# Kernel optimization log

Measured on AMD Instinct MI355X. Metric: run time of the kernel, lower is better.

Reference implementation:

```python
import jax, jax.numpy as jnp
from jax import lax
import numpy as np

INPUT_SIZE, HIDDEN_SIZE, OUTPUT_SIZE = 256, 2048, 128
NUM_STEPS = 8192
ALPHA = 0.1


def setup_inputs() -> dict:
    key = jax.random.key(0)
    ks = jax.random.split(key, 8)
    s_i = 1.0 / np.sqrt(INPUT_SIZE)
    s_h = 1.0 / np.sqrt(HIDDEN_SIZE)
    return {
        "input_sig": jax.random.normal(ks[0], (INPUT_SIZE, NUM_STEPS), jnp.float32),
        "rate": jax.random.uniform(ks[1], (HIDDEN_SIZE,), jnp.float32, -1.0, 1.0),
        "Wi": jax.random.uniform(ks[2], (HIDDEN_SIZE, INPUT_SIZE), jnp.float32, -s_i, s_i),
        "bi": jax.random.uniform(ks[3], (HIDDEN_SIZE,), jnp.float32, -s_i, s_i),
        "Wh": jax.random.uniform(ks[4], (HIDDEN_SIZE, HIDDEN_SIZE), jnp.float32, -s_h, s_h),
        "bh": jax.random.uniform(ks[5], (HIDDEN_SIZE,), jnp.float32, -s_h, s_h),
        "Wo": jax.random.uniform(ks[6], (OUTPUT_SIZE, HIDDEN_SIZE), jnp.float32, -s_h, s_h),
        "bo": jax.random.uniform(ks[7], (OUTPUT_SIZE,), jnp.float32, -s_h, s_h),
    }


def reference(input_sig, rate, Wi, bi, Wh, bh, Wo, bo):
    # Precompute input projection for all steps at once: (T, H)
    xproj = input_sig.T @ Wi.T + bi  # einsum 'ti,hi->th'

    def step(r, xp):
        r_new = jnp.tanh(xp + r @ Wh.T + bh)
        r = (1.0 - ALPHA) * r + ALPHA * r_new
        return r, r

    _, rates = lax.scan(step, rate, xproj)  # rates: (T, H)
    rate_all = rates.T                      # (H, T), matches torch stack(dim=1)
    logits = rates @ Wo.T + bo              # (T, O)
    output = jax.nn.log_softmax(logits.T, axis=0)  # LogSoftmax over classes
    return output, rate_all
```

## Files before the change

### kernel.cpp

```cpp
#include <hip/hip_runtime.h>
#include <math.h>

#define T_STEPS 8192
#define HID     2048
#define IN_SZ   256
#define OUT_SZ  128
#define NBLK    128
#define NTHR    512
#define RPB     16
#define SCRUB   0xFFFFFFFF00000000ull

typedef unsigned long long u64;
typedef unsigned int u32;
typedef __attribute__((ext_vector_type(4))) u32 u32x4;


__global__ void k_init(const float* __restrict__ rate, u64* ring) {
    int i = blockIdx.x * blockDim.x + threadIdx.x;
    if (i < HID) {
        ring[i] = (u64)__float_as_uint(rate[i]);
        ring[HID + i]     = SCRUB;
        ring[2 * HID + i] = SCRUB;
    }
}

__global__ void __launch_bounds__(256) k_xproj(const float* __restrict__ sig,
                                               const float* __restrict__ Wi,
                                               const float* __restrict__ bi,
                                               float* __restrict__ out2) {
    __shared__ float wl[32 * IN_SZ];
    const int tid = threadIdx.x;
    const int t0 = blockIdx.x * 512;
    const int h0 = blockIdx.y * 32;

    {
        const float4* s4 = (const float4*)(Wi + (size_t)h0 * IN_SZ);
        float4* d4 = (float4*)wl;
        #pragma unroll
        for (int k = 0; k < 8; ++k) d4[tid + k * 256] = s4[tid + k * 256];
    }
    __syncthreads();

    const int t1 = t0 + tid, t2 = t1 + 256;
    float acc1[32], acc2[32];
    #pragma unroll
    for (int j = 0; j < 32; ++j) { acc1[j] = 0.f; acc2[j] = 0.f; }

    for (int i = 0; i < IN_SZ; ++i) {
        float s1 = sig[(size_t)i * T_STEPS + t1];
        float s2 = sig[(size_t)i * T_STEPS + t2];
        #pragma unroll
        for (int j = 0; j < 32; ++j) {
            float w = wl[j * IN_SZ + i];
            acc1[j] = fmaf(w, s1, acc1[j]);
            acc2[j] = fmaf(w, s2, acc2[j]);
        }
    }
    #pragma unroll
    for (int j = 0; j < 32; ++j) {
        float b = bi[h0 + j];
        out2[(size_t)(h0 + j) * T_STEPS + t1] = acc1[j] + b;
        out2[(size_t)(h0 + j) * T_STEPS + t2] = acc2[j] + b;
    }
}

#define DECLROW(p) \
    float p##_0,  p##_1,  p##_2,  p##_3,  p##_4,  p##_5,  p##_6,  p##_7,  \
          p##_8,  p##_9,  p##_10, p##_11, p##_12, p##_13, p##_14, p##_15, \
          p##_16, p##_17, p##_18, p##_19, p##_20, p##_21, p##_22, p##_23, \
          p##_24, p##_25, p##_26, p##_27, p##_28, p##_29, p##_30, p##_31

#define SCAT(v, a, b, c, d) a = (v).x; b = (v).y; c = (v).z; d = (v).w

#define PIN8(a,b,c,d,e,f,g,h) \
    asm volatile("" : "+v"(a), "+v"(b), "+v"(c), "+v"(d), \
                      "+v"(e), "+v"(f), "+v"(g), "+v"(h))

#define PINROW(p) \
    PIN8(p##_0,  p##_1,  p##_2,  p##_3,  p##_4,  p##_5,  p##_6,  p##_7);  \
    PIN8(p##_8,  p##_9,  p##_10, p##_11, p##_12, p##_13, p##_14, p##_15); \
    PIN8(p##_16, p##_17, p##_18, p##_19, p##_20, p##_21, p##_22, p##_23); \
    PIN8(p##_24, p##_25, p##_26, p##_27, p##_28, p##_29, p##_30, p##_31)

#define LOADROW(p, base) { \
    float4 v; \
    v = (base)[0 * 64 + lane]; SCAT(v, p##_0,  p##_1,  p##_2,  p##_3);  \
    v = (base)[1 * 64 + lane]; SCAT(v, p##_4,  p##_5,  p##_6,  p##_7);  \
    v = (base)[2 * 64 + lane]; SCAT(v, p##_8,  p##_9,  p##_10, p##_11); \
    v = (base)[3 * 64 + lane]; SCAT(v, p##_12, p##_13, p##_14, p##_15); \
    v = (base)[4 * 64 + lane]; SCAT(v, p##_16, p##_17, p##_18, p##_19); \
    v = (base)[5 * 64 + lane]; SCAT(v, p##_20, p##_21, p##_22, p##_23); \
    v = (base)[6 * 64 + lane]; SCAT(v, p##_24, p##_25, p##_26, p##_27); \
    v = (base)[7 * 64 + lane]; SCAT(v, p##_28, p##_29, p##_30, p##_31); }

#define DOTC(c, s0, s1, s2, s3) { \
    float4 rv = r4[(c) * 64 + lane]; \
    p0 = fmaf(rv.x, wa_##s0, p0); p0 = fmaf(rv.y, wa_##s1, p0); \
    p0 = fmaf(rv.z, wa_##s2, p0); p0 = fmaf(rv.w, wa_##s3, p0); \
    p1 = fmaf(rv.x, wb_##s0, p1); p1 = fmaf(rv.y, wb_##s1, p1); \
    p1 = fmaf(rv.z, wb_##s2, p1); p1 = fmaf(rv.w, wb_##s3, p1); }

__global__ void __launch_bounds__(512, 2) k_scan(const float* __restrict__ Wh,
                                                 const float* __restrict__ bh,
                                                 float* __restrict__ out2,
                                                 u64* ring) {
    __shared__ float rl[HID];
    const int tid  = threadIdx.x;
    const int bid  = blockIdx.x;
    const int w    = tid >> 6;
    const int lane = tid & 63;
    const int h0   = bid * RPB;
    const int ra   = h0 + 2 * w;

    const float4* Wh4 = (const float4*)Wh;
    DECLROW(wa);
    DECLROW(wb);
    LOADROW(wa, Wh4 + (size_t)ra * 512);
    LOADROW(wb, Wh4 + (size_t)(ra + 1) * 512);
    PINROW(wa);
    PINROW(wb);

    const int myrow = ra + lane;
    float mybh = 0.f;
    if (lane < 2) mybh = bh[myrow];
    __syncthreads();

    int cur = 0;
    for (int t = 0; t < T_STEPS; ++t) {
        float xp = 0.f;
        size_t myidx = 0;
        if (lane < 2) {
            myidx = (size_t)myrow * T_STEPS + t;
            xp = out2[myidx];
        }

        {
            const u64* src = ring + (size_t)cur * HID;
            const u64* p0p = src + 4 * tid;
            const u64* p1p = p0p + 2;
            const u32 tt = (u32)t;
            u32x4 a0, a1;
            float f0, f1, f2, f3;
            int got = 0;
            for (int rounds = 0; rounds < 32; ++rounds) {
                asm volatile("global_load_dwordx4 %0, %2, off sc1\n\t"
                             "global_load_dwordx4 %1, %3, off sc1\n\t"
                             "s_waitcnt vmcnt(0)"
                             : "=&v"(a0), "=&v"(a1)
                             : "v"(p0p), "v"(p1p)
                             : "memory");
                __builtin_amdgcn_sched_barrier(0);
                if (a0.y == tt && a0.w == tt && a1.y == tt && a1.w == tt) {
                    f0 = __uint_as_float(a0.x);
                    f1 = __uint_as_float(a0.z);
                    f2 = __uint_as_float(a1.x);
                    f3 = __uint_as_float(a1.z);
                    got = 1;
                    break;
                }
            }
            if (!got) {
                u64 vals[4];
                unsigned pend = 0xFu;
                while (pend) {
                    #pragma unroll
                    for (int q = 0; q < 4; ++q) {
                        if (pend & (1u << q))
                            vals[q] = __hip_atomic_load(&p0p[q], __ATOMIC_RELAXED,
                                                        __HIP_MEMORY_SCOPE_AGENT);
                    }
                    #pragma unroll
                    for (int q = 0; q < 4; ++q) {
                        if ((pend & (1u << q)) && (u32)(vals[q] >> 32) == tt)
                            pend &= ~(1u << q);
                    }
                }
                f0 = __uint_as_float((u32)vals[0]);
                f1 = __uint_as_float((u32)vals[1]);
                f2 = __uint_as_float((u32)vals[2]);
                f3 = __uint_as_float((u32)vals[3]);
            }
            float4 v; v.x = f0; v.y = f1; v.z = f2; v.w = f3;
            ((float4*)rl)[tid] = v;
        }
        __syncthreads();

        float p0 = 0.f, p1 = 0.f;
        {
            const float4* r4 = (const float4*)rl;
            DOTC(0, 0,  1,  2,  3);
            DOTC(1, 4,  5,  6,  7);
            DOTC(2, 8,  9,  10, 11);
            DOTC(3, 12, 13, 14, 15);
            DOTC(4, 16, 17, 18, 19);
            DOTC(5, 20, 21, 22, 23);
            DOTC(6, 24, 25, 26, 27);
            DOTC(7, 28, 29, 30, 31);
        }
        #pragma unroll
        for (int off = 32; off >= 1; off >>= 1) {
            p0 += __shfl_xor(p0, off, 64);
            p1 += __shfl_xor(p1, off, 64);
        }

        const int nxt = (cur == 2) ? 0 : cur + 1;
        if (lane < 2) {
            float myp = (lane & 1) ? p1 : p0;
            float rold = rl[myrow];
            float v = myp + xp + mybh;
            float rn = 0.9f * rold + 0.1f * tanhf(v);
            out2[myidx] = rn;
            u64* dst = ring + (size_t)nxt * HID;
            const u64 tagbits = (u64)(u32)(t + 1) << 32;
            __hip_atomic_store(&dst[myrow], tagbits | __float_as_uint(rn),
                               __ATOMIC_RELAXED, __HIP_MEMORY_SCOPE_AGENT);
        }
        cur = nxt;
    }
}

__global__ void __launch_bounds__(512) k_logits(const float* __restrict__ out2,
                                                const float* __restrict__ Wo,
                                                const float* __restrict__ bo,
                                                float* __restrict__ out0) {
    __shared__ float wos[128 * 128];
    __shared__ float red[8 * 128];
    __shared__ float fin[128];
    const int tid  = threadIdx.x;
    const int w    = tid >> 6;
    const int lane = tid & 63;
    const int t0   = blockIdx.x * 128;
    const int ob   = w * 16;

    float acc0[16], acc1[16];
    #pragma unroll
    for (int j = 0; j < 16; ++j) { acc0[j] = 0.f; acc1[j] = 0.f; }

    for (int hb = 0; hb < HID / 128; ++hb) {
        __syncthreads();
        {
            const float4* wo4 = (const float4*)Wo;
            float4* ws4 = (float4*)wos;
            #pragma unroll
            for (int k = 0; k < 8; ++k) {
                int g = tid + k * 512;
                int o = g >> 5;
                int c = g & 31;
                ws4[g] = wo4[(size_t)o * (HID / 4) + hb * 32 + c];
            }
        }
        __syncthreads();
        for (int hh = 0; hh < 128; ++hh) {
            int h = hb * 128 + hh;
            float rA = out2[(size_t)h * T_STEPS + t0 + lane];
            float rB = out2[(size_t)h * T_STEPS + t0 + 64 + lane];
            #pragma unroll
            for (int j = 0; j < 16; ++j) {
                float wv = wos[(ob + j) * 128 + hh];
                acc0[j] = fmaf(wv, rA, acc0[j]);
                acc1[j] = fmaf(wv, rB, acc1[j]);
            }
        }
    }
    #pragma unroll
    for (int j = 0; j < 16; ++j) {
        float b = bo[ob + j];
        acc0[j] += b; acc1[j] += b;
    }

    float m0 = acc0[0], m1 = acc1[0];
    #pragma unroll
    for (int j = 1; j < 16; ++j) { m0 = fmaxf(m0, acc0[j]); m1 = fmaxf(m1, acc1[j]); }
    red[w * 128 + lane] = m0;
    red[w * 128 + 64 + lane] = m1;
    __syncthreads();
    if (tid < 128) {
        float m = red[tid];
        #pragma unroll
        for (int q = 1; q < 8; ++q) m = fmaxf(m, red[q * 128 + tid]);
        fin[tid] = m;
    }
    __syncthreads();
    float fm0 = fin[lane], fm1 = fin[64 + lane];
    float s0 = 0.f, s1 = 0.f;
    #pragma unroll
    for (int j = 0; j < 16; ++j) {
        s0 += expf(acc0[j] - fm0);
        s1 += expf(acc1[j] - fm1);
    }
    red[w * 128 + lane] = s0;
    red[w * 128 + 64 + lane] = s1;
    __syncthreads();
    if (tid < 128) {
        float s = 0.f;
        #pragma unroll
        for (int q = 0; q < 8; ++q) s += red[q * 128 + tid];
        fin[tid] = fin[tid] + logf(s);
    }
    __syncthreads();
    float L0 = fin[lane], L1 = fin[64 + lane];
    #pragma unroll
    for (int j = 0; j < 16; ++j) {
        out0[(size_t)(ob + j) * T_STEPS + t0 + lane]      = acc0[j] - L0;
        out0[(size_t)(ob + j) * T_STEPS + t0 + 64 + lane] = acc1[j] - L1;
    }
}

extern "C" void kernel_launch(void* const* d_in, const int* in_sizes, int n_in,
                              void* d_out, int out_size, void* d_ws, size_t ws_size,
                              hipStream_t stream) {
    const float* sig  = (const float*)d_in[0];
    const float* rate = (const float*)d_in[1];
    const float* Wi   = (const float*)d_in[2];
    const float* bi   = (const float*)d_in[3];
    const float* Wh   = (const float*)d_in[4];
    const float* bh   = (const float*)d_in[5];
    const float* Wo   = (const float*)d_in[6];
    const float* bo   = (const float*)d_in[7];

    float* out0 = (float*)d_out;
    float* out2 = out0 + (size_t)OUT_SZ * T_STEPS;

    u64* ring = (u64*)d_ws;

    hipLaunchKernelGGL(k_init, dim3(8), dim3(256), 0, stream, rate, ring);
    hipLaunchKernelGGL(k_xproj, dim3(T_STEPS / 512, HID / 32), dim3(256), 0, stream,
                       sig, Wi, bi, out2);

    void* args[] = {(void*)&Wh, (void*)&bh, (void*)&out2, (void*)&ring};
    hipLaunchCooperativeKernel((const void*)k_scan, dim3(NBLK), dim3(NTHR),
                               args, 0, stream);

    hipLaunchKernelGGL(k_logits, dim3(T_STEPS / 128), dim3(512), 0, stream,
                       out2, Wo, bo, out0);
}
```

Baseline: 15.19 ms.

## Halve scan blocks to 64 with four rows per wave and double-buffered LDS

The recurrent scan now runs on 64 blocks instead of 128, each wave owning four Wh rows held in registers rather than two. Shared rate storage becomes double-buffered by step parity. The aim is to halve the number of participants in the per-step cross-block ring synchronization and cut polling traffic, at the cost of twice the per-wave FMA work and register pressure, with a risk of spilling 128 pinned weights per thread.

```diff
diff --git a/kernel.cpp b/kernel.cpp
--- a/kernel.cpp
+++ b/kernel.cpp
@@ -5,9 +5,9 @@
 #define HID     2048
 #define IN_SZ   256
 #define OUT_SZ  128
-#define NBLK    128
+#define NBLK    64
 #define NTHR    512
-#define RPB     16
+#define RPB     32
 #define SCRUB   0xFFFFFFFF00000000ull
 
 typedef unsigned long long u64;
@@ -93,43 +93,54 @@
     v = (base)[6 * 64 + lane]; SCAT(v, p##_24, p##_25, p##_26, p##_27); \
     v = (base)[7 * 64 + lane]; SCAT(v, p##_28, p##_29, p##_30, p##_31); }
 
-#define DOTC(c, s0, s1, s2, s3) { \
+#define DOTC4(c, s0, s1, s2, s3) { \
     float4 rv = r4[(c) * 64 + lane]; \
     p0 = fmaf(rv.x, wa_##s0, p0); p0 = fmaf(rv.y, wa_##s1, p0); \
     p0 = fmaf(rv.z, wa_##s2, p0); p0 = fmaf(rv.w, wa_##s3, p0); \
     p1 = fmaf(rv.x, wb_##s0, p1); p1 = fmaf(rv.y, wb_##s1, p1); \
-    p1 = fmaf(rv.z, wb_##s2, p1); p1 = fmaf(rv.w, wb_##s3, p1); }
+    p1 = fmaf(rv.z, wb_##s2, p1); p1 = fmaf(rv.w, wb_##s3, p1); \
+    p2 = fmaf(rv.x, wc_##s0, p2); p2 = fmaf(rv.y, wc_##s1, p2); \
+    p2 = fmaf(rv.z, wc_##s2, p2); p2 = fmaf(rv.w, wc_##s3, p2); \
+    p3 = fmaf(rv.x, wd_##s0, p3); p3 = fmaf(rv.y, wd_##s1, p3); \
+    p3 = fmaf(rv.z, wd_##s2, p3); p3 = fmaf(rv.w, wd_##s3, p3); }
 
 __global__ void __launch_bounds__(512, 2) k_scan(const float* __restrict__ Wh,
                                                  const float* __restrict__ bh,
                                                  float* __restrict__ out2,
                                                  u64* ring) {
-    __shared__ float rl[HID];
+    __shared__ float rl[2][HID];
     const int tid  = threadIdx.x;
     const int bid  = blockIdx.x;
     const int w    = tid >> 6;
     const int lane = tid & 63;
     const int h0   = bid * RPB;
-    const int ra   = h0 + 2 * w;
+    const int ra   = h0 + 4 * w;
 
     const float4* Wh4 = (const float4*)Wh;
     DECLROW(wa);
     DECLROW(wb);
+    DECLROW(wc);
+    DECLROW(wd);
     LOADROW(wa, Wh4 + (size_t)ra * 512);
     LOADROW(wb, Wh4 + (size_t)(ra + 1) * 512);
+    LOADROW(wc, Wh4 + (size_t)(ra + 2) * 512);
+    LOADROW(wd, Wh4 + (size_t)(ra + 3) * 512);
     PINROW(wa);
     PINROW(wb);
+    PINROW(wc);
+    PINROW(wd);
 
     const int myrow = ra + lane;
     float mybh = 0.f;
-    if (lane < 2) mybh = bh[myrow];
+    if (lane < 4) mybh = bh[myrow];
     __syncthreads();
 
     int cur = 0;
     for (int t = 0; t < T_STEPS; ++t) {
+        const int buf = t & 1;
         float xp = 0.f;
         size_t myidx = 0;
-        if (lane < 2) {
+        if (lane < 4) {
             myidx = (size_t)myrow * T_STEPS + t;
             xp = out2[myidx];
         }
@@ -181,32 +192,35 @@
                 f3 = __uint_as_float((u32)vals[3]);
             }
             float4 v; v.x = f0; v.y = f1; v.z = f2; v.w = f3;
-            ((float4*)rl)[tid] = v;
+            ((float4*)rl[buf])[tid] = v;
         }
         __syncthreads();
 
-        float p0 = 0.f, p1 = 0.f;
+        float p0 = 0.f, p1 = 0.f, p2 = 0.f, p3 = 0.f;
         {
-            const float4* r4 = (const float4*)rl;
-            DOTC(0, 0,  1,  2,  3);
-            DOTC(1, 4,  5,  6,  7);
-            DOTC(2, 8,  9,  10, 11);
-            DOTC(3, 12, 13, 14, 15);
-            DOTC(4, 16, 17, 18, 19);
-            DOTC(5, 20, 21, 22, 23);
-            DOTC(6, 24, 25, 26, 27);
-            DOTC(7, 28, 29, 30, 31);
+            const float4* r4 = (const float4*)rl[buf];
+            DOTC4(0, 0,  1,  2,  3);
+            DOTC4(1, 4,  5,  6,  7);
+            DOTC4(2, 8,  9,  10, 11);
+            DOTC4(3, 12, 13, 14, 15);
+            DOTC4(4, 16, 17, 18, 19);
+            DOTC4(5, 20, 21, 22, 23);
+            DOTC4(6, 24, 25, 26, 27);
+            DOTC4(7, 28, 29, 30, 31);
         }
         #pragma unroll
         for (int off = 32; off >= 1; off >>= 1) {
             p0 += __shfl_xor(p0, off, 64);
             p1 += __shfl_xor(p1, off, 64);
+            p2 += __shfl_xor(p2, off, 64);
+            p3 += __shfl_xor(p3, off, 64);
         }
 
         const int nxt = (cur == 2) ? 0 : cur + 1;
-        if (lane < 2) {
-            float myp = (lane & 1) ? p1 : p0;
-            float rold = rl[myrow];
+        if (lane < 4) {
+            float myp = (lane & 2) ? ((lane & 1) ? p3 : p2)
+                                   : ((lane & 1) ? p1 : p0);
+            float rold = rl[buf][myrow];
             float v = myp + xp + mybh;
             float rn = 0.9f * rold + 0.1f * tanhf(v);
             out2[myidx] = rn;
```

Result: slower. 17.09 ms (+12.5%).
